# Optimization experiments

Hardware: AMD Instinct MI355X
Metric: run time of the kernel (lower is better)

The kernel has to match this reference:

```python
import jax, jax.numpy as jnp
import numpy as np

L_MAX = 5
C_IN = 24
HIDDEN = 32
BATCH = 256


def _valid_pairs(l):
    return [(l1, l2) for l1 in range(L_MAX + 1) for l2 in range(L_MAX + 1)
            if abs(l1 - l2) <= l <= l1 + l2]


def _make_cg():
    # Packed padded CG coefficient tensor cg[l1, l2, l, m, m1, m2].
    # Values are fixed deterministic constants; sparsity follows the true
    # selection rule m = m1 + m2 (indices stored shifted by +l).
    D = 2 * L_MAX + 1
    rng = np.random.RandomState(42)
    cg = np.zeros((L_MAX + 1, L_MAX + 1, L_MAX + 1, D, D, D), dtype=np.float32)
    for l in range(L_MAX + 1):
        for (l1, l2) in _valid_pairs(l):
            m = np.arange(-l, l + 1)[:, None, None]
            m1 = np.arange(-l1, l1 + 1)[None, :, None]
            m2 = np.arange(-l2, l2 + 1)[None, None, :]
            mask = (m == m1 + m2).astype(np.float32)
            vals = rng.randn(2 * l + 1, 2 * l1 + 1, 2 * l2 + 1).astype(np.float32)
            cg[l1, l2, l, :2 * l + 1, :2 * l1 + 1, :2 * l2 + 1] = vals * mask
    return jnp.asarray(cg)


def setup_inputs() -> dict:
    key = jax.random.key(0)
    keys = jax.random.split(key, 12)
    inp = {}
    for l in range(L_MAX + 1):
        inp[f"x{l}"] = jax.random.normal(keys[l], (BATCH, C_IN, 2 * l + 1), dtype=jnp.float32)
    for l in range(L_MAX + 1):
        k_in = len(_valid_pairs(l)) * C_IN * C_IN
        scale = 1.0 / np.sqrt(k_in)
        inp[f"W{l}"] = jax.random.normal(keys[6 + l], (HIDDEN, k_in), dtype=jnp.float32) * scale
    inp["cg"] = _make_cg()
    return inp


def reference(x0, x1, x2, x3, x4, x5, W0, W1, W2, W3, W4, W5, cg):
    xs = [x0, x1, x2, x3, x4, x5]
    Ws = [W0, W1, W2, W3, W4, W5]
    outs = []
    for l in range(L_MAX + 1):
        feats = []
        for (l1, l2) in _valid_pairs(l):
            c = cg[l1, l2, l, :2 * l + 1, :2 * l1 + 1, :2 * l2 + 1]  # [2l+1, 2l1+1, 2l2+1]
            # P[b, c1, c2, m] = sum_{m1,m2} cg[m,m1,m2] x_l1[b,c1,m1] x_l2[b,c2,m2]
            p = jnp.einsum('mij,bci,bdj->bcdm', c, xs[l1], xs[l2])
            feats.append(p.reshape(p.shape[0], -1, 2 * l + 1))
        cat = jnp.concatenate(feats, axis=1)  # [B, n_pairs*C*C, 2l+1]
        outs.append(jnp.einsum('hk,bkm->bhm', Ws[l], cat))  # [B, HIDDEN, 2l+1]
    # concat orders along the m axis -> [B, HIDDEN, sum_l (2l+1) = 36]
    return jnp.concatenate(outs, axis=-1)
```

## Files before the change

### kernel.cpp

```cpp
#include <hip/hip_runtime.h>
#include <hip/hip_bf16.h>

typedef __attribute__((ext_vector_type(8))) short bf16x8;
typedef __attribute__((ext_vector_type(4))) float f32x4;
typedef __attribute__((ext_vector_type(2))) float f32x2;

struct Params {
  const float* x[6];
  const float* W[6];
  const float* cg;
  float* out;
  unsigned short* Wb;
};

constexpr int NPAIRS_C[6] = {6, 15, 21, 24, 24, 21};
constexpr int POFF_C[6]   = {0, 6, 21, 42, 66, 90};
constexpr size_t WBASE_C[6] = {0, 110592, 387072, 774144, 1216512, 1658880};
constexpr int KL_C[6]   = {3456, 8640, 12096, 13824, 13824, 12096};
#define XSTRIDE 236
#define BSTRIDE 28

__constant__ int c_l1[111] = {
  0,1,2,3,4,5,
  0,1,1,1,2,2,2,3,3,3,4,4,4,5,5,
  0,1,1,1,2,2,2,2,2,3,3,3,3,3,4,4,4,4,5,5,5,
  0,1,1,1,2,2,2,2,2,3,3,3,3,3,3,4,4,4,4,4,5,5,5,5,
  0,1,1,1,2,2,2,2,3,3,3,3,3,4,4,4,4,4,4,5,5,5,5,5,
  0,1,1,2,2,2,3,3,3,3,4,4,4,4,4,5,5,5,5,5,5
};
__constant__ int c_l2[111] = {
  0,1,2,3,4,5,
  1,0,1,2,1,2,3,2,3,4,3,4,5,4,5,
  2,1,2,3,0,1,2,3,4,1,2,3,4,5,2,3,4,5,3,4,5,
  3,2,3,4,1,2,3,4,5,0,1,2,3,4,5,1,2,3,4,5,2,3,4,5,
  4,3,4,5,2,3,4,5,1,2,3,4,5,0,1,2,3,4,5,1,2,3,4,5,
  5,4,5,3,4,5,2,3,4,5,1,2,3,4,5,0,1,2,3,4,5
};
__constant__ int c_loff[6] = {0, 1, 4, 9, 16, 25};
__constant__ int c_mb_l[21]  = {5,5,5,5,5,5, 4,4,4,4,4, 3,3,3,3, 2,2,2, 1,1, 0};
__constant__ int c_mb_m0[21] = {0,2,4,6,8,10, 0,2,4,6,8, 0,2,4,6, 0,2,4, 0,2, 0};
__constant__ int c_GA3[6] = {0,1,2,9,10,11};

template<int L>
__device__ __forceinline__ void swz(const Params& P, int u8) {
  constexpr int KL = KL_C[L];
  constexpr int KL8 = KL / 8;
  if (u8 >= 32 * KL8) return;
  const int h  = u8 / KL8;
  const int k  = (u8 - h * KL8) * 8;
  const int pair = k / 576;
  const int kin  = k - pair * 576;
  const int kc = kin >> 5;
  const int g  = (kin >> 3) & 3;
  const float* src = P.W[L] + (size_t)h * KL + k;
  f32x4 v0 = *(const f32x4*)src;
  f32x4 v1 = *(const f32x4*)(src + 4);
  union { __hip_bfloat162 h2; unsigned int u; } z;
  unsigned int o0, o1, o2, o3;
  z.h2 = __float22bfloat162_rn(make_float2(v0.x, v0.y)); o0 = z.u;
  z.h2 = __float22bfloat162_rn(make_float2(v0.z, v0.w)); o1 = z.u;
  z.h2 = __float22bfloat162_rn(make_float2(v1.x, v1.y)); o2 = z.u;
  z.h2 = __float22bfloat162_rn(make_float2(v1.z, v1.w)); o3 = z.u;
  const size_t dst = WBASE_C[L] + (size_t)pair * 18432 + kc * 1024 + (h >> 4) * 512
                   + ((size_t)(g * 16 + (h & 15))) * 8;
  *(uint4*)(P.Wb + dst) = make_uint4(o0, o1, o2, o3);
}

__global__ __launch_bounds__(256)
void swizzle_W(Params P) {
  const int u8 = blockIdx.x * 256 + threadIdx.x;
  switch (blockIdx.y) {
    case 0: swz<0>(P, u8); break;
    case 1: swz<1>(P, u8); break;
    case 2: swz<2>(P, u8); break;
    case 3: swz<3>(P, u8); break;
    case 4: swz<4>(P, u8); break;
    default: swz<5>(P, u8); break;
  }
}

#define XALL_F 0
#define CG_F   8968
#define SMEM_FLOATS 9544

template<int L>
__device__ __forceinline__ void body(const Params& P, const int mp0, const int btile,
                                     const int half) {
  constexpr int NP  = NPAIRS_C[L];
  constexpr int OFF = POFF_C[L];
  extern __shared__ float smem[];
  float* xall  = smem + XALL_F;
  float* cgall = smem + CG_F;
  float* red   = smem + XALL_F;

  const int t    = threadIdx.x;
  const int lane = t & 63;
  const int w    = t >> 6;
  const int q8   = lane >> 4;
  const int rI   = lane & 15;
  const int b    = rI & 7;
  const int mpL  = rI >> 3;
  const int b0   = btile * 8;
  const int p0   = half ? NP / 2 : 0;
  const int p1   = half ? NP : NP / 2;

  for (int e = t; e < 2 * XSTRIDE; e += 384) {
    const int r = (e < XSTRIDE) ? 0 : 37;
    xall[r * XSTRIDE + (e % XSTRIDE)] = 0.f;
  }
#pragma unroll
  for (int l = 0; l < 6; ++l) {
    const int n = 2 * l + 1;
    const float* src = P.x[l] + (size_t)b0 * 24 * n;
    const int tot = 8 * 24 * n;
    for (int e = t; e < tot; e += 384) {
      const int bc = e / n;
      const int i  = e - bc * n;
      const int bb = bc / 24;
      const int cc = bc - 24 * bb;
      xall[(1 + c_loff[l] + i) * XSTRIDE + bb * BSTRIDE + cc] = src[e];
    }
  }
  for (int e = t; e < 2 * NP * 12; e += 384) {
    const int i  = e % 12;
    const int r  = e / 12;
    const int pi = r % NP;
    const int mL = r / NP;
    const int l1 = c_l1[OFF + pi], l2 = c_l2[OFF + pi];
    const int mp = mp0 + mL;
    const int j  = mp + l1 + l2 - L - i;
    float v = 0.f;
    if (mp <= 2 * L && i <= 2 * l1 && j >= 0 && j <= 2 * l2)
      v = P.cg[((size_t)(((l1 * 6 + l2) * 6 + L) * 11 + mp) * 11 + i) * 11 + j];
    cgall[(mL * NP + pi) * 12 + i] = v;
  }
  __syncthreads();

  f32x4 accC0 = {0.f, 0.f, 0.f, 0.f};
  f32x4 accC1 = {0.f, 0.f, 0.f, 0.f};

  const int kcA = c_GA3[w];
  const int k0  = kcA * 32 + q8 * 8;
  const int cA  = k0 / 24;
  const int d0  = k0 - cA * 24;
  const int bcol = b * BSTRIDE;
  const float* x2l = xall + (size_t)(1 + mpL) * XSTRIDE + bcol + d0;
  const float* x1l = xall + (size_t)1 * XSTRIDE + bcol + cA;

  for (int pi = p0; pi < p1; ++pi) {
    const int l1 = c_l1[OFF + pi], l2 = c_l2[OFF + pi];
    const int n1 = 2 * l1 + 1, n2 = 2 * l2 + 1;
    const int R1 = c_loff[l1], R2 = c_loff[l2];
    const int mK0w = mp0 + l1 + l2 - L;
    const int lo = mK0w - (n2 - 1);
    const int i0 = lo > 0 ? lo : 0;
    const int i1 = (n1 - 1) < (mK0w + 1) ? (n1 - 1) : (mK0w + 1);

    const unsigned short* wbp = P.Wb + WBASE_C[L] + (size_t)pi * 18432 + lane * 8;
    const bf16x8 wfA0 = *(const bf16x8*)(wbp + kcA * 1024);
    const bf16x8 wfA1 = *(const bf16x8*)(wbp + kcA * 1024 + 512);
    const bf16x8 wfB0 = *(const bf16x8*)(wbp + (kcA + 3) * 1024);
    const bf16x8 wfB1 = *(const bf16x8*)(wbp + (kcA + 3) * 1024 + 512);
    const bf16x8 wfC0 = *(const bf16x8*)(wbp + (kcA + 6) * 1024);
    const bf16x8 wfC1 = *(const bf16x8*)(wbp + (kcA + 6) * 1024 + 512);

    f32x2 pA[4], pB[4], pC[4];
#pragma unroll
    for (int dd = 0; dd < 4; ++dd) {
      pA[dd] = (f32x2){0.f, 0.f};
      pB[dd] = (f32x2){0.f, 0.f};
      pC[dd] = (f32x2){0.f, 0.f};
    }

    const float* cgp = cgall + (mpL * NP + pi) * 12 + i0;
    const float* x2p = x2l + (size_t)(R2 + mK0w - i0) * XSTRIDE;
    const float* x1p = x1l + (size_t)(R1 + i0) * XSTRIDE;
    for (int i = i0; i <= i1; ++i) {
      const float cgv = *cgp++;
      f32x2 xv[4];
      *(f32x4*)&xv[0] = *(const f32x4*)x2p;
      *(f32x4*)&xv[2] = *(const f32x4*)(x2p + 4);
      const float sA = cgv * x1p[0];
      const float sB = cgv * x1p[4];
      const float sC = cgv * x1p[8];
      x2p -= XSTRIDE; x1p += XSTRIDE;
      const f32x2 svA = {sA, sA}, svB = {sB, sB}, svC = {sC, sC};
#pragma unroll
      for (int dd = 0; dd < 4; ++dd) {
        pA[dd] += svA * xv[dd];
        pB[dd] += svB * xv[dd];
        pC[dd] += svC * xv[dd];
      }
    }
    union { unsigned int u[4]; bf16x8 v; } zA, zB, zC;
#pragma unroll
    for (int dd = 0; dd < 4; ++dd) {
      union { __hip_bfloat162 h2; unsigned int u; } z;
      z.h2 = __float22bfloat162_rn(make_float2(pA[dd].x, pA[dd].y)); zA.u[dd] = z.u;
      z.h2 = __float22bfloat162_rn(make_float2(pB[dd].x, pB[dd].y)); zB.u[dd] = z.u;
      z.h2 = __float22bfloat162_rn(make_float2(pC[dd].x, pC[dd].y)); zC.u[dd] = z.u;
    }
    accC0 = __builtin_amdgcn_mfma_f32_16x16x32_bf16(zA.v, wfA0, accC0, 0, 0, 0);
    accC0 = __builtin_amdgcn_mfma_f32_16x16x32_bf16(zB.v, wfB0, accC0, 0, 0, 0);
    accC0 = __builtin_amdgcn_mfma_f32_16x16x32_bf16(zC.v, wfC0, accC0, 0, 0, 0);
    accC1 = __builtin_amdgcn_mfma_f32_16x16x32_bf16(zA.v, wfA1, accC1, 0, 0, 0);
    accC1 = __builtin_amdgcn_mfma_f32_16x16x32_bf16(zB.v, wfB1, accC1, 0, 0, 0);
    accC1 = __builtin_amdgcn_mfma_f32_16x16x32_bf16(zC.v, wfC1, accC1, 0, 0, 0);
  }

  __syncthreads();
  {
    const int col16 = lane & 15;
    const int rbase = w * 16 + (lane >> 4) * 4;
#pragma unroll
    for (int r = 0; r < 4; ++r) {
      red[(rbase + r) * 32 + col16]      = accC0[r];
      red[(rbase + r) * 32 + 16 + col16] = accC1[r];
    }
  }
  __syncthreads();
  for (int idx = t; idx < 512; idx += 384) {
    const int row = idx >> 5, h = idx & 31;
    float v = 0.f;
#pragma unroll
    for (int ww = 0; ww < 6; ++ww) v += red[ww * 512 + row * 32 + h];
    const int ob = row & 7, omL = row >> 3;
    const int mp = mp0 + omL;
    if (mp <= 2 * L)
      atomicAdd(&P.out[(size_t)(b0 + ob) * 1152 + h * 36 + L * L + mp], v);
  }
}

__global__ __launch_bounds__(384, 5)
void CGLayer_main(Params P) {
  const int mb = blockIdx.x;
  const int l = c_mb_l[mb], mp0 = c_mb_m0[mb];
  const int btile = blockIdx.y >> 1;
  const int half  = blockIdx.y & 1;
  switch (l) {
    case 0: body<0>(P, mp0, btile, half); break;
    case 1: body<1>(P, mp0, btile, half); break;
    case 2: body<2>(P, mp0, btile, half); break;
    case 3: body<3>(P, mp0, btile, half); break;
    case 4: body<4>(P, mp0, btile, half); break;
    default: body<5>(P, mp0, btile, half); break;
  }
}

extern "C" void kernel_launch(void* const* d_in, const int* in_sizes, int n_in,
                              void* d_out, int out_size, void* d_ws, size_t ws_size,
                              hipStream_t stream) {
  Params P;
  for (int i = 0; i < 6; ++i) P.x[i] = (const float*)d_in[i];
  for (int i = 0; i < 6; ++i) P.W[i] = (const float*)d_in[6 + i];
  P.cg  = (const float*)d_in[12];
  P.out = (float*)d_out;
  P.Wb  = (unsigned short*)d_ws;

  hipMemsetAsync(d_out, 0, (size_t)out_size * sizeof(float), stream);
  dim3 sg(216, 6);
  swizzle_W<<<sg, 256, 0, stream>>>(P);
  dim3 grid(21, 64);
  CGLayer_main<<<grid, 384, SMEM_FLOATS * sizeof(float), stream>>>(P);
}
```

Measured before the change: 161.7 us.

## Retile CG blocks to 4 batches by 4 orders, drop pair split and atomics

Each block now covers 4 batch rows and 4 output orders (m) instead of 8 batches and 2 orders, and loops over all CG pairs instead of half of them. Grid shrinks from 21x64 to 12x64. Because a block now owns its whole output tile, results are written with plain stores, which removes the output memset and the atomicAdd traffic. The smaller shared footprint allows a higher occupancy bound. The cost is that each block streams all W fragments per pair for fewer batches, which raises weight reuse pressure, and fewer blocks means less parallelism.

New measurement: 149.7 us. 1.08x faster.

```diff
diff --git a/kernel.cpp b/kernel.cpp
--- a/kernel.cpp
+++ b/kernel.cpp
@@ -17,8 +17,9 @@
 constexpr int POFF_C[6]   = {0, 6, 21, 42, 66, 90};
 constexpr size_t WBASE_C[6] = {0, 110592, 387072, 774144, 1216512, 1658880};
 constexpr int KL_C[6]   = {3456, 8640, 12096, 13824, 13824, 12096};
-#define XSTRIDE 236
+#define XSTRIDE 116
 #define BSTRIDE 28
+#define NGUARD 3
 
 __constant__ int c_l1[111] = {
   0,1,2,3,4,5,
@@ -37,8 +38,8 @@
   5,4,5,3,4,5,2,3,4,5,1,2,3,4,5,0,1,2,3,4,5
 };
 __constant__ int c_loff[6] = {0, 1, 4, 9, 16, 25};
-__constant__ int c_mb_l[21]  = {5,5,5,5,5,5, 4,4,4,4,4, 3,3,3,3, 2,2,2, 1,1, 0};
-__constant__ int c_mb_m0[21] = {0,2,4,6,8,10, 0,2,4,6,8, 0,2,4,6, 0,2,4, 0,2, 0};
+__constant__ int c_mb_l[12]  = {4,4,4, 3,3, 5,5,5, 2,2, 1, 0};
+__constant__ int c_mb_m0[12] = {0,4,8, 0,4, 0,4,8, 0,4, 0, 0};
 __constant__ int c_GA3[6] = {0,1,2,9,10,11};
 
 template<int L>
@@ -80,12 +81,11 @@
 }
 
 #define XALL_F 0
-#define CG_F   8968
-#define SMEM_FLOATS 9544
+#define CG_F   4872
+#define SMEM_FLOATS 6024
 
 template<int L>
-__device__ __forceinline__ void body(const Params& P, const int mp0, const int btile,
-                                     const int half) {
+__device__ __forceinline__ void body(const Params& P, const int mp0, const int btile) {
   constexpr int NP  = NPAIRS_C[L];
   constexpr int OFF = POFF_C[L];
   extern __shared__ float smem[];
@@ -98,30 +98,29 @@
   const int w    = t >> 6;
   const int q8   = lane >> 4;
   const int rI   = lane & 15;
-  const int b    = rI & 7;
-  const int mpL  = rI >> 3;
-  const int b0   = btile * 8;
-  const int p0   = half ? NP / 2 : 0;
-  const int p1   = half ? NP : NP / 2;
-
-  for (int e = t; e < 2 * XSTRIDE; e += 384) {
-    const int r = (e < XSTRIDE) ? 0 : 37;
-    xall[r * XSTRIDE + (e % XSTRIDE)] = 0.f;
+  const int b    = rI & 3;
+  const int mpL  = rI >> 2;
+  const int b0   = btile * 4;
+
+  for (int e = t; e < 6 * XSTRIDE; e += 384) {
+    const int r = e / XSTRIDE;
+    const int row = (r < 3) ? r : 36 + r;
+    xall[row * XSTRIDE + (e - r * XSTRIDE)] = 0.f;
   }
 #pragma unroll
   for (int l = 0; l < 6; ++l) {
     const int n = 2 * l + 1;
     const float* src = P.x[l] + (size_t)b0 * 24 * n;
-    const int tot = 8 * 24 * n;
+    const int tot = 4 * 24 * n;
     for (int e = t; e < tot; e += 384) {
       const int bc = e / n;
       const int i  = e - bc * n;
       const int bb = bc / 24;
       const int cc = bc - 24 * bb;
-      xall[(1 + c_loff[l] + i) * XSTRIDE + bb * BSTRIDE + cc] = src[e];
-    }
-  }
-  for (int e = t; e < 2 * NP * 12; e += 384) {
+      xall[(NGUARD + c_loff[l] + i) * XSTRIDE + bb * BSTRIDE + cc] = src[e];
+    }
+  }
+  for (int e = t; e < 4 * NP * 12; e += 384) {
     const int i  = e % 12;
     const int r  = e / 12;
     const int pi = r % NP;
@@ -144,17 +143,17 @@
   const int cA  = k0 / 24;
   const int d0  = k0 - cA * 24;
   const int bcol = b * BSTRIDE;
-  const float* x2l = xall + (size_t)(1 + mpL) * XSTRIDE + bcol + d0;
-  const float* x1l = xall + (size_t)1 * XSTRIDE + bcol + cA;
-
-  for (int pi = p0; pi < p1; ++pi) {
+  const float* x2l = xall + (size_t)(NGUARD + mpL) * XSTRIDE + bcol + d0;
+  const float* x1l = xall + (size_t)NGUARD * XSTRIDE + bcol + cA;
+
+  for (int pi = 0; pi < NP; ++pi) {
     const int l1 = c_l1[OFF + pi], l2 = c_l2[OFF + pi];
     const int n1 = 2 * l1 + 1, n2 = 2 * l2 + 1;
     const int R1 = c_loff[l1], R2 = c_loff[l2];
     const int mK0w = mp0 + l1 + l2 - L;
     const int lo = mK0w - (n2 - 1);
     const int i0 = lo > 0 ? lo : 0;
-    const int i1 = (n1 - 1) < (mK0w + 1) ? (n1 - 1) : (mK0w + 1);
+    const int i1 = (n1 - 1) < (mK0w + 3) ? (n1 - 1) : (mK0w + 3);
 
     const unsigned short* wbp = P.Wb + WBASE_C[L] + (size_t)pi * 18432 + lane * 8;
     const bf16x8 wfA0 = *(const bf16x8*)(wbp + kcA * 1024);
@@ -224,26 +223,25 @@
     float v = 0.f;
 #pragma unroll
     for (int ww = 0; ww < 6; ++ww) v += red[ww * 512 + row * 32 + h];
-    const int ob = row & 7, omL = row >> 3;
+    const int ob = row & 3, omL = row >> 2;
     const int mp = mp0 + omL;
     if (mp <= 2 * L)
-      atomicAdd(&P.out[(size_t)(b0 + ob) * 1152 + h * 36 + L * L + mp], v);
-  }
-}
-
-__global__ __launch_bounds__(384, 5)
+      P.out[(size_t)(b0 + ob) * 1152 + h * 36 + L * L + mp] = v;
+  }
+}
+
+__global__ __launch_bounds__(384, 6)
 void CGLayer_main(Params P) {
   const int mb = blockIdx.x;
   const int l = c_mb_l[mb], mp0 = c_mb_m0[mb];
-  const int btile = blockIdx.y >> 1;
-  const int half  = blockIdx.y & 1;
+  const int btile = blockIdx.y;
   switch (l) {
-    case 0: body<0>(P, mp0, btile, half); break;
-    case 1: body<1>(P, mp0, btile, half); break;
-    case 2: body<2>(P, mp0, btile, half); break;
-    case 3: body<3>(P, mp0, btile, half); break;
-    case 4: body<4>(P, mp0, btile, half); break;
-    default: body<5>(P, mp0, btile, half); break;
+    case 0: body<0>(P, mp0, btile); break;
+    case 1: body<1>(P, mp0, btile); break;
+    case 2: body<2>(P, mp0, btile); break;
+    case 3: body<3>(P, mp0, btile); break;
+    case 4: body<4>(P, mp0, btile); break;
+    default: body<5>(P, mp0, btile); break;
   }
 }
 
@@ -257,9 +255,8 @@
   P.out = (float*)d_out;
   P.Wb  = (unsigned short*)d_ws;
 
-  hipMemsetAsync(d_out, 0, (size_t)out_size * sizeof(float), stream);
   dim3 sg(216, 6);
   swizzle_W<<<sg, 256, 0, stream>>>(P);
-  dim3 grid(21, 64);
+  dim3 grid(12, 64);
   CGLayer_main<<<grid, 384, SMEM_FLOATS * sizeof(float), stream>>>(P);
 }
```
